# Kernel optimization log

Hardware: AMD Instinct MI355X
Metric: run time of the kernel (lower is better)

Reference implementation:

```python
import jax, jax.numpy as jnp
import numpy as np

N_HEAD = 8
D_K = 64
D_V = 512
TOP_K = 64
NEG = jnp.finfo(jnp.float32).min


def setup_inputs() -> dict:
    key = jax.random.key(0)
    ks = jax.random.split(key, 10)
    B, Lq, Lk, E = 2, 2048, 2048, 512
    q = jax.random.normal(ks[0], (B, Lq, E), dtype=jnp.float32)
    k = jax.random.normal(ks[1], (B, Lk, E), dtype=jnp.float32)
    v = jax.random.normal(ks[2], (B, Lk, D_V), dtype=jnp.float32)
    post_softmax_mask = jax.random.randint(ks[3], (B, 1, Lq, Lk), 0, 2, dtype=jnp.int32)
    query_mask_flat = jax.random.uniform(ks[4], (B, Lq), dtype=jnp.float32)
    # Linear weights stored input-major: y = x @ W
    Wq = jax.random.normal(ks[5], (E, N_HEAD * D_K), dtype=jnp.float32) * (E ** -0.5)
    Wk = jax.random.normal(ks[6], (E, N_HEAD * D_K), dtype=jnp.float32) * (E ** -0.5)
    Wv = jax.random.normal(ks[7], (D_V, N_HEAD * D_V), dtype=jnp.float32) * (D_V ** -0.5)
    Wfc = jax.random.normal(ks[8], (N_HEAD * D_V, D_V), dtype=jnp.float32) * ((N_HEAD * D_V) ** -0.5)
    return {"q": q, "k": k, "v": v, "post_softmax_mask": post_softmax_mask,
            "query_mask_flat": query_mask_flat, "Wq": Wq, "Wk": Wk, "Wv": Wv, "Wfc": Wfc}


def _topk_keep_mask(logits, top_k):
    # Scatter True at the per-row top-k indices (matches torch.topk + scatter_).
    B, H, Lq, Lk = logits.shape
    _, idx = jax.lax.top_k(logits, top_k)              # [B,H,Lq,K]
    rows = B * H * Lq
    keep = jnp.zeros((rows, Lk), dtype=bool)
    keep = keep.at[jnp.arange(rows)[:, None], idx.reshape(rows, top_k)].set(True)
    return keep.reshape(B, H, Lq, Lk)


def reference(q, k, v, post_softmax_mask, query_mask_flat, Wq, Wk, Wv, Wfc):
    B, Lq, _ = q.shape
    Lk = k.shape[1]
    q_proj = (q @ Wq).reshape(B, Lq, N_HEAD, D_K).transpose(0, 2, 1, 3)   # [B,H,Lq,dk]
    k_proj = (k @ Wk).reshape(B, Lk, N_HEAD, D_K).transpose(0, 2, 1, 3)   # [B,H,Lk,dk]
    logits = jnp.einsum('bhqd,bhkd->bhqk', q_proj * (D_K ** -0.5), k_proj).astype(jnp.float32)
    # post-softmax mask (applied pre-softmax via -inf fill, as in source)
    logits = jnp.where(post_softmax_mask == 0, NEG, logits)
    # top-k restriction, skipped for rows where query_mask_flat <= 0.5
    keep = _topk_keep_mask(logits, TOP_K)
    masked_queries = (query_mask_flat > 0.5)[:, None, :, None]            # [B,1,Lq,1]
    keep = jnp.where(masked_queries, keep, True)
    logits = jnp.where(keep, logits, NEG)
    attn_probs = jax.nn.softmax(logits, axis=-1).astype(v.dtype)          # [B,H,Lq,Lk]
    v_proj = (v @ Wv).reshape(B, Lk, N_HEAD, D_V).transpose(0, 2, 1, 3)   # [B,H,Lk,dv]
    mixed = jnp.einsum('bhqk,bhkd->bhqd', attn_probs, v_proj)
    output = mixed.transpose(0, 2, 1, 3).reshape(B, Lq, N_HEAD * D_V) @ Wfc
    return output, attn_probs
```

## Files before the change

### kernel.cpp

```cpp
#include <hip/hip_runtime.h>
#include <stdint.h>

#define NEGF  (-3.402823466e38f)
#define TOPK  64

typedef __attribute__((ext_vector_type(8))) short bfrag8;
typedef __attribute__((ext_vector_type(4))) float f32x4;
typedef __attribute__((ext_vector_type(16))) float f32x16;

static __device__ __forceinline__ unsigned short f2bf(float f) {
  union { float f; unsigned u; } c; c.f = f;
  unsigned u = c.u;
  return (unsigned short)((u + 0x7fffu + ((u >> 16) & 1u)) >> 16);
}
static __device__ __forceinline__ unsigned mono(float x) {
  union { float f; unsigned u; } c; c.f = x;
  return (c.u & 0x80000000u) ? ~c.u : (c.u | 0x80000000u);
}
static __device__ __forceinline__ float invmono(unsigned k) {
  union { unsigned u; float f; } c;
  c.u = (k & 0x80000000u) ? (k ^ 0x80000000u) : ~k;
  return c.f;
}
static __device__ __forceinline__ int waveSum(int v) {
  #pragma unroll
  for (int o = 1; o < 64; o <<= 1) v += __shfl_xor(v, o);
  return v;
}
static __device__ __forceinline__ float waveSumF(float v) {
  #pragma unroll
  for (int o = 1; o < 64; o <<= 1) v += __shfl_xor(v, o);
  return v;
}
static __device__ __forceinline__ unsigned waveMaxU(unsigned v) {
  #pragma unroll
  for (int o = 1; o < 64; o <<= 1) {
    unsigned t = (unsigned)__shfl_xor((int)v, o);
    v = v > t ? v : t;
  }
  return v;
}

template<int OBF>
__global__ __launch_bounds__(256) void transpose_k(const float* __restrict__ in,
                                                   void* __restrict__ out, int R, int C) {
  __shared__ float t[32][33];
  int c0 = blockIdx.x * 32, r0 = blockIdx.y * 32;
  int tx = threadIdx.x & 31, ty = (threadIdx.x >> 5) * 4;
  #pragma unroll
  for (int i = 0; i < 4; i++)
    t[ty + i][tx] = in[(size_t)(r0 + ty + i) * C + c0 + tx];
  __syncthreads();
  #pragma unroll
  for (int i = 0; i < 4; i++) {
    float v = t[tx][ty + i];
    size_t idx = (size_t)(c0 + ty + i) * R + r0 + tx;
    if (OBF) ((unsigned short*)out)[idx] = f2bf(v);
    else     ((float*)out)[idx] = v;
  }
}

__global__ __launch_bounds__(256) void gemm_f32_abt(const float* __restrict__ A,
    const float* __restrict__ Bt, float* __restrict__ C,
    int M, int N, int K, float scale) {
  __shared__ float As[64][65];
  __shared__ float Bs[64][65];
  int tid = threadIdx.x;
  int tx = tid & 15, ty = tid >> 4;
  int m0 = blockIdx.y * 64, n0 = blockIdx.x * 64;
  float acc[4][4] = {};
  for (int k0 = 0; k0 < K; k0 += 64) {
    #pragma unroll
    for (int i = 0; i < 4; i++) {
      int f = tid + (i << 8);
      int row = f >> 4, kc = (f & 15) << 2;
      float4 av = *(const float4*)(A + (size_t)(m0 + row) * K + k0 + kc);
      As[row][kc+0] = av.x; As[row][kc+1] = av.y; As[row][kc+2] = av.z; As[row][kc+3] = av.w;
      float4 bv = *(const float4*)(Bt + (size_t)(n0 + row) * K + k0 + kc);
      Bs[row][kc+0] = bv.x; Bs[row][kc+1] = bv.y; Bs[row][kc+2] = bv.z; Bs[row][kc+3] = bv.w;
    }
    __syncthreads();
    #pragma unroll 4
    for (int d = 0; d < 64; d++) {
      float a[4], b[4];
      #pragma unroll
      for (int i = 0; i < 4; i++) a[i] = As[ty*4 + i][d];
      #pragma unroll
      for (int j = 0; j < 4; j++) b[j] = Bs[tx*4 + j][d];
      #pragma unroll
      for (int i = 0; i < 4; i++)
        #pragma unroll
        for (int j = 0; j < 4; j++)
          acc[i][j] = fmaf(a[i], b[j], acc[i][j]);
    }
    __syncthreads();
  }
  #pragma unroll
  for (int i = 0; i < 4; i++) {
    int m = m0 + ty*4 + i;
    float4 v4;
    v4.x = acc[i][0]*scale; v4.y = acc[i][1]*scale; v4.z = acc[i][2]*scale; v4.w = acc[i][3]*scale;
    int b = m >> 11, l = m & 2047;
    int n = n0 + tx*4;
    int h = n >> 6, dd = n & 63;
    *(float4*)(C + ((((size_t)b*8 + h)*2048 + l)*64 + dd)) = v4;
  }
}

__global__ __launch_bounds__(256) void logits_mask_kernel(
    const float* __restrict__ qp, const float* __restrict__ kp,
    const int* __restrict__ mask, float* __restrict__ out) {
  __shared__ float AsT[64][132];
  __shared__ float BsT[64][132];
  int tid = threadIdx.x;
  int z = blockIdx.z, b = z >> 3;
  int m0 = blockIdx.y * 128, n0 = blockIdx.x * 128;
  const float* Ap = qp + (size_t)z * (2048 * 64);
  const float* Bp = kp + (size_t)z * (2048 * 64);
  {
    int rr = tid >> 2;
    int kq = (tid & 3) << 2;
    #pragma unroll
    for (int pass = 0; pass < 2; pass++) {
      int r = rr + (pass << 6);
      const float* ar = Ap + (size_t)(m0 + r) * 64 + kq;
      const float* br = Bp + (size_t)(n0 + r) * 64 + kq;
      #pragma unroll
      for (int s = 0; s < 4; s++) {
        float4 av = *(const float4*)(ar + (s << 4));
        float4 bv = *(const float4*)(br + (s << 4));
        int k = kq + (s << 4);
        AsT[k+0][r] = av.x; AsT[k+1][r] = av.y; AsT[k+2][r] = av.z; AsT[k+3][r] = av.w;
        BsT[k+0][r] = bv.x; BsT[k+1][r] = bv.y; BsT[k+2][r] = bv.z; BsT[k+3][r] = bv.w;
      }
    }
  }
  __syncthreads();
  int lane = tid & 63, w = tid >> 6;
  int lx = lane & 15, ly = lane >> 4;
  int ra = w * 32 + ly * 4;
  int ca = lx * 4;
  float acc[8][8] = {};
  #pragma unroll 2
  for (int d = 0; d < 64; d++) {
    f32x4 a0 = *(const f32x4*)&AsT[d][ra];
    f32x4 a1 = *(const f32x4*)&AsT[d][ra + 16];
    f32x4 b0 = *(const f32x4*)&BsT[d][ca];
    f32x4 b1 = *(const f32x4*)&BsT[d][ca + 64];
    float a[8] = {a0[0],a0[1],a0[2],a0[3],a1[0],a1[1],a1[2],a1[3]};
    float bb[8] = {b0[0],b0[1],b0[2],b0[3],b1[0],b1[1],b1[2],b1[3]};
    #pragma unroll
    for (int i = 0; i < 8; i++)
      #pragma unroll
      for (int j = 0; j < 8; j++)
        acc[i][j] = fmaf(a[i], bb[j], acc[i][j]);
  }
  size_t outbase = (size_t)z * 2048 * 2048;
  const int* mbase = mask + (size_t)b * 2048 * 2048;
  #pragma unroll
  for (int i = 0; i < 8; i++) {
    int row = m0 + ra + (i & 3) + ((i >> 2) << 4);
    const int* mp = mbase + (size_t)row * 2048 + n0;
    float* op = out + outbase + (size_t)row * 2048 + n0;
    int4 mv0 = *(const int4*)(mp + ca);
    int4 mv1 = *(const int4*)(mp + ca + 64);
    float4 o0, o1;
    o0.x = mv0.x ? acc[i][0] : NEGF;
    o0.y = mv0.y ? acc[i][1] : NEGF;
    o0.z = mv0.z ? acc[i][2] : NEGF;
    o0.w = mv0.w ? acc[i][3] : NEGF;
    o1.x = mv1.x ? acc[i][4] : NEGF;
    o1.y = mv1.y ? acc[i][5] : NEGF;
    o1.z = mv1.z ? acc[i][6] : NEGF;
    o1.w = mv1.w ? acc[i][7] : NEGF;
    *(float4*)(op + ca) = o0;
    *(float4*)(op + ca + 64) = o1;
  }
}

template<typename AT, int MODE>
__global__ __launch_bounds__(256) void gemm_bf16(const AT* __restrict__ A,
    const unsigned short* __restrict__ Bt, void* __restrict__ Cout,
    int M, int N, int K) {
  __shared__ unsigned short As[64][72];
  __shared__ unsigned short Bs[128][72];
  int tid = threadIdx.x;
  int lane = tid & 63, wave = tid >> 6;
  int wr = wave >> 1, wc = wave & 1;
  int m0 = blockIdx.y * 64, n0 = blockIdx.x * 128;
  f32x4 acc[2][4];
  #pragma unroll
  for (int mi = 0; mi < 2; mi++)
    #pragma unroll
    for (int ni = 0; ni < 4; ni++) acc[mi][ni] = (f32x4){0.f, 0.f, 0.f, 0.f};
  int arow = tid >> 2, akc = (tid & 3) << 4;
  int brow = tid >> 1, bkc = (tid & 1) << 5;
  for (int k0 = 0; k0 < K; k0 += 64) {
    {
      const AT* src = A + (size_t)(m0 + arow) * K + k0 + akc;
      if constexpr (sizeof(AT) == 4) {
        const float* s = (const float*)src;
        float4 x0 = *(const float4*)(s + 0);
        float4 x1 = *(const float4*)(s + 4);
        float4 x2 = *(const float4*)(s + 8);
        float4 x3 = *(const float4*)(s + 12);
        union { bfrag8 v; unsigned short u[8]; } p0, p1;
        p0.u[0]=f2bf(x0.x); p0.u[1]=f2bf(x0.y); p0.u[2]=f2bf(x0.z); p0.u[3]=f2bf(x0.w);
        p0.u[4]=f2bf(x1.x); p0.u[5]=f2bf(x1.y); p0.u[6]=f2bf(x1.z); p0.u[7]=f2bf(x1.w);
        p1.u[0]=f2bf(x2.x); p1.u[1]=f2bf(x2.y); p1.u[2]=f2bf(x2.z); p1.u[3]=f2bf(x2.w);
        p1.u[4]=f2bf(x3.x); p1.u[5]=f2bf(x3.y); p1.u[6]=f2bf(x3.z); p1.u[7]=f2bf(x3.w);
        *(bfrag8*)&As[arow][akc + 0] = p0.v;
        *(bfrag8*)&As[arow][akc + 8] = p1.v;
      } else {
        const bfrag8* s = (const bfrag8*)src;
        *(bfrag8*)&As[arow][akc + 0] = s[0];
        *(bfrag8*)&As[arow][akc + 8] = s[1];
      }
    }
    {
      const bfrag8* s = (const bfrag8*)(Bt + (size_t)(n0 + brow) * K + k0 + bkc);
      #pragma unroll
      for (int j = 0; j < 4; j++)
        *(bfrag8*)&Bs[brow][bkc + 8*j] = s[j];
    }
    __syncthreads();
    #pragma unroll
    for (int kh = 0; kh < 2; kh++) {
      int krd = (kh << 5) + ((lane >> 4) << 3);
      bfrag8 af[2], bfr[4];
      #pragma unroll
      for (int mi = 0; mi < 2; mi++)
        af[mi] = *(const bfrag8*)&As[wr*32 + mi*16 + (lane & 15)][krd];
      #pragma unroll
      for (int ni = 0; ni < 4; ni++)
        bfr[ni] = *(const bfrag8*)&Bs[wc*64 + ni*16 + (lane & 15)][krd];
      #pragma unroll
      for (int mi = 0; mi < 2; mi++)
        #pragma unroll
        for (int ni = 0; ni < 4; ni++)
          acc[mi][ni] = __builtin_amdgcn_mfma_f32_16x16x32_bf16(af[mi], bfr[ni], acc[mi][ni], 0, 0, 0);
    }
    __syncthreads();
  }
  #pragma unroll
  for (int mi = 0; mi < 2; mi++) {
    int rb = m0 + wr*32 + mi*16 + ((lane >> 4) << 2);
    #pragma unroll
    for (int ni = 0; ni < 4; ni++) {
      int col = n0 + wc*64 + ni*16 + (lane & 15);
      f32x4 v = acc[mi][ni];
      if (MODE == 0) {
        int b = rb >> 11, l = rb & 2047;
        int h = col >> 9, d = col & 511;
        unsigned short* o = (unsigned short*)Cout + ((((size_t)b*8 + h)*512 + d)*2048 + l);
        ushort4 u;
        u.x = f2bf(v[0]); u.y = f2bf(v[1]); u.z = f2bf(v[2]); u.w = f2bf(v[3]);
        *(ushort4*)o = u;
      } else {
        float* o = (float*)Cout;
        #pragma unroll
        for (int j = 0; j < 4; j++)
          o[(size_t)(rb + j)*512 + col] = v[j];
      }
    }
  }
}

__global__ __launch_bounds__(512) void pv_kernel(const float* __restrict__ probs,
    const unsigned short* __restrict__ vpT, unsigned short* __restrict__ mixed) {
  __shared__ unsigned short As[64][64];
  __shared__ unsigned short Bs[512][64];
  int tid = threadIdx.x;
  int lane = tid & 63, wv = tid >> 6;
  int l31 = lane & 31, lh = lane >> 5;
  int z = blockIdx.z, m0 = blockIdx.y * 64;
  const float* Ap = probs + (size_t)z * 2048 * 2048 + (size_t)m0 * 2048;
  const unsigned short* Bp = vpT + (size_t)z * 512 * 2048;
  f32x16 acc[2][2];
  #pragma unroll
  for (int mf = 0; mf < 2; mf++)
    #pragma unroll
    for (int nf = 0; nf < 2; nf++)
      #pragma unroll
      for (int r = 0; r < 16; r++) acc[mf][nf][r] = 0.f;
  int a_r = tid >> 3, a_c = tid & 7;
  for (int k0 = 0; k0 < 2048; k0 += 64) {
    {
      const float* s = Ap + (size_t)a_r * 2048 + k0 + a_c * 8;
      float4 x0 = *(const float4*)s;
      float4 x1 = *(const float4*)(s + 4);
      union { bfrag8 v; unsigned short u[8]; } p;
      p.u[0]=f2bf(x0.x); p.u[1]=f2bf(x0.y); p.u[2]=f2bf(x0.z); p.u[3]=f2bf(x0.w);
      p.u[4]=f2bf(x1.x); p.u[5]=f2bf(x1.y); p.u[6]=f2bf(x1.z); p.u[7]=f2bf(x1.w);
      *(bfrag8*)&As[a_r][((a_c + a_r) & 7) * 8] = p.v;
    }
    #pragma unroll
    for (int s = 0; s < 8; s++) {
      int n = (tid >> 3) + (s << 6);
      bfrag8 vb = *(const bfrag8*)(Bp + (size_t)n * 2048 + k0 + a_c * 8);
      *(bfrag8*)&Bs[n][((a_c + n) & 7) * 8] = vb;
    }
    __syncthreads();
    #pragma unroll
    for (int ks = 0; ks < 4; ks++) {
      int qd = ks * 2 + lh;
      bfrag8 af[2], bfr[2];
      #pragma unroll
      for (int mf = 0; mf < 2; mf++) {
        int r = mf * 32 + l31;
        af[mf] = *(const bfrag8*)&As[r][((qd + r) & 7) * 8];
      }
      #pragma unroll
      for (int nf = 0; nf < 2; nf++) {
        int n = wv * 64 + nf * 32 + l31;
        bfr[nf] = *(const bfrag8*)&Bs[n][((qd + n) & 7) * 8];
      }
      #pragma unroll
      for (int mf = 0; mf < 2; mf++)
        #pragma unroll
        for (int nf = 0; nf < 2; nf++)
          acc[mf][nf] = __builtin_amdgcn_mfma_f32_32x32x16_bf16(af[mf], bfr[nf], acc[mf][nf], 0, 0, 0);
    }
    __syncthreads();
  }
  int bb = z >> 3, h = z & 7;
  #pragma unroll
  for (int mf = 0; mf < 2; mf++)
    #pragma unroll
    for (int nf = 0; nf < 2; nf++) {
      int n = wv * 64 + nf * 32 + l31;
      #pragma unroll
      for (int r = 0; r < 16; r++) {
        int row = m0 + mf * 32 + (r & 3) + ((r >> 2) << 3) + (lh << 2);
        mixed[((size_t)bb * 2048 + row) * 4096 + h * 512 + n] = f2bf(acc[mf][nf][r]);
      }
    }
}

__global__ __launch_bounds__(256) void topk_softmax_k(float* __restrict__ probs,
    const float* __restrict__ qmaskf) {
  int lane = threadIdx.x & 63;
  int row = blockIdx.x * 4 + (threadIdx.x >> 6);
  int b = row >> 14, q = row & 2047;
  float* rp = probs + (size_t)row * 2048;
  unsigned key[32];
  #pragma unroll
  for (int j = 0; j < 8; j++) {
    int base = (lane << 2) + (j << 8);
    float4 v = *(const float4*)(rp + base);
    key[4*j+0] = mono(v.x);
    key[4*j+1] = mono(v.y);
    key[4*j+2] = mono(v.z);
    key[4*j+3] = mono(v.w);
  }
  unsigned drop = 0;
  bool qm = qmaskf[b * 2048 + q] > 0.5f;
  if (qm) {
    unsigned lo = 0u, hi = 0xFFFFu;
    while (lo < hi) {
      unsigned mid = lo + ((hi - lo + 1u) >> 1);
      unsigned t = mid << 16;
      int c = 0;
      #pragma unroll
      for (int e = 0; e < 32; e++) c += (key[e] >= t) ? 1 : 0;
      c = waveSum(c);
      if (c >= TOPK) lo = mid; else hi = mid - 1u;
    }
    unsigned P = lo;
    unsigned hiMax = (P << 16) | 0xFFFFu;
    int cgt_hi = 0;
    #pragma unroll
    for (int e = 0; e < 32; e++) cgt_hi += (key[e] > hiMax) ? 1 : 0;
    cgt_hi = waveSum(cgt_hi);
    int remaining = TOPK - cgt_hi;
    unsigned cur = 0xFFFFFFFFu;
    unsigned K64 = P << 16;
    for (;;) {
      unsigned mx = 0;
      #pragma unroll
      for (int e = 0; e < 32; e++) {
        unsigned kk = key[e];
        if ((kk >> 16) == P && kk < cur) mx = mx > kk ? mx : kk;
      }
      mx = waveMaxU(mx);
      int ce = 0;
      #pragma unroll
      for (int e = 0; e < 32; e++) ce += (key[e] == mx) ? 1 : 0;
      ce = waveSum(ce);
      if (remaining <= ce) { K64 = mx; break; }
      remaining -= ce;
      cur = mx;
    }
    int cgt = 0, ceq = 0;
    #pragma unroll
    for (int e = 0; e < 32; e++) { cgt += (key[e] > K64) ? 1 : 0; ceq += (key[e] == K64) ? 1 : 0; }
    cgt = waveSum(cgt);
    int ceqT = waveSum(ceq);
    int r = TOPK - cgt;
    #pragma unroll
    for (int e = 0; e < 32; e++) if (key[e] < K64) drop |= (1u << e);
    if (ceqT > r) {
      int taken = 0;
      for (int j = 0; j < 8; j++) {
        int cl = 0, eqm = 0;
        #pragma unroll
        for (int t = 0; t < 4; t++)
          if (key[4*j+t] == K64) { eqm |= (1 << t); cl++; }
        int incl = cl;
        for (int o = 1; o < 64; o <<= 1) {
          int tt = __shfl_up(incl, o);
          if (lane >= o) incl += tt;
        }
        int pref = incl - cl;
        int tot = __shfl(incl, 63);
        int rk = taken + pref;
        #pragma unroll
        for (int t = 0; t < 4; t++) {
          if ((eqm >> t) & 1) {
            if (rk >= r) drop |= (1u << (4*j+t));
            rk++;
          }
        }
        taken += tot;
      }
    }
  }
  unsigned kmax = 0;
  #pragma unroll
  for (int e = 0; e < 32; e++)
    if (!((drop >> e) & 1u)) kmax = kmax > key[e] ? kmax : key[e];
  kmax = waveMaxU(kmax);
  float mx = invmono(kmax);
  float ex[32]; float s = 0.f;
  #pragma unroll
  for (int e = 0; e < 32; e++) {
    float t = ((drop >> e) & 1u) ? 0.f : __expf(invmono(key[e]) - mx);
    ex[e] = t; s += t;
  }
  s = waveSumF(s);
  float inv = 1.0f / s;
  #pragma unroll
  for (int j = 0; j < 8; j++) {
    int base = (lane << 2) + (j << 8);
    float4 o;
    o.x = ex[4*j+0]*inv; o.y = ex[4*j+1]*inv; o.z = ex[4*j+2]*inv; o.w = ex[4*j+3]*inv;
    *(float4*)(rp + base) = o;
  }
}

extern "C" void kernel_launch(void* const* d_in, const int* in_sizes, int n_in,
                              void* d_out, int out_size, void* d_ws, size_t ws_size,
                              hipStream_t stream) {
  (void)in_sizes; (void)n_in; (void)out_size; (void)ws_size;
  const float* q     = (const float*)d_in[0];
  const float* k     = (const float*)d_in[1];
  const float* v     = (const float*)d_in[2];
  const int*   mask  = (const int*)d_in[3];
  const float* qmask = (const float*)d_in[4];
  const float* Wq    = (const float*)d_in[5];
  const float* Wk    = (const float*)d_in[6];
  const float* Wv    = (const float*)d_in[7];
  const float* Wfc   = (const float*)d_in[8];

  float* out   = (float*)d_out;
  float* probs = out + 2097152;

  char* ws = (char*)d_ws;
  float*          qp    = (float*)(ws + 0);
  float*          kp    = (float*)(ws + 8388608);
  unsigned short* vpT   = (unsigned short*)(ws + 16777216);
  unsigned short* mixed = (unsigned short*)(ws + 50331648);
  float*          WqT   = (float*)(ws + 83886080);
  float*          WkT   = (float*)(ws + 84934656);
  unsigned short* WvT   = (unsigned short*)(ws + 85983232);
  unsigned short* WfcT  = (unsigned short*)(ws + 90177536);

  transpose_k<0><<<dim3(16, 16),  256, 0, stream>>>(Wq,  WqT,  512, 512);
  transpose_k<0><<<dim3(16, 16),  256, 0, stream>>>(Wk,  WkT,  512, 512);
  transpose_k<1><<<dim3(128, 16), 256, 0, stream>>>(Wv,  WvT,  512, 4096);
  transpose_k<1><<<dim3(16, 128), 256, 0, stream>>>(Wfc, WfcT, 4096, 512);

  gemm_f32_abt<<<dim3(8, 64), 256, 0, stream>>>(q, WqT, qp, 4096, 512, 512, 0.125f);
  gemm_f32_abt<<<dim3(8, 64), 256, 0, stream>>>(k, WkT, kp, 4096, 512, 512, 1.0f);

  gemm_bf16<float, 0><<<dim3(32, 64), 256, 0, stream>>>(v, WvT, vpT, 4096, 4096, 512);

  logits_mask_kernel<<<dim3(16, 16, 16), 256, 0, stream>>>(qp, kp, mask, probs);

  topk_softmax_k<<<dim3(8192), 256, 0, stream>>>(probs, qmask);

  pv_kernel<<<dim3(1, 32, 16), 512, 0, stream>>>(probs, vpT, mixed);

  gemm_bf16<unsigned short, 2><<<dim3(4, 64), 256, 0, stream>>>(mixed, WfcT, out, 4096, 512, 4096);
}
```

Measured before the change: 588.7 us.

## Merge Q/K projections into one larger-tile kernel and rewrite V projection with 32x32 MFMA

Replaces the two separate fp32 Q and K projection launches with a single kernel that handles both via blockIdx.z. It uses 128x128 tiles with an 8x8 per-thread register block and transposed shared-memory staging. The V projection gets its own kernel that computes the transposed output directly with 32x32x16 bf16 MFMA, 128x128 tiles and XOR-style swizzled shared memory. The aim is more arithmetic per load and fewer launches, but the V output stores are scalar and strided, which may cost bandwidth.

```diff
diff --git a/kernel.cpp b/kernel.cpp
--- a/kernel.cpp
+++ b/kernel.cpp
@@ -60,50 +60,67 @@
   }
 }
 
-__global__ __launch_bounds__(256) void gemm_f32_abt(const float* __restrict__ A,
-    const float* __restrict__ Bt, float* __restrict__ C,
-    int M, int N, int K, float scale) {
-  __shared__ float As[64][65];
-  __shared__ float Bs[64][65];
+__global__ __launch_bounds__(256) void proj_f32_kernel(
+    const float* __restrict__ q, const float* __restrict__ k,
+    const float* __restrict__ WqT, const float* __restrict__ WkT,
+    float* __restrict__ qp, float* __restrict__ kp) {
+  __shared__ float AsT[64][132];
+  __shared__ float BsT[64][132];
   int tid = threadIdx.x;
-  int tx = tid & 15, ty = tid >> 4;
-  int m0 = blockIdx.y * 64, n0 = blockIdx.x * 64;
-  float acc[4][4] = {};
-  for (int k0 = 0; k0 < K; k0 += 64) {
-    #pragma unroll
-    for (int i = 0; i < 4; i++) {
-      int f = tid + (i << 8);
-      int row = f >> 4, kc = (f & 15) << 2;
-      float4 av = *(const float4*)(A + (size_t)(m0 + row) * K + k0 + kc);
-      As[row][kc+0] = av.x; As[row][kc+1] = av.y; As[row][kc+2] = av.z; As[row][kc+3] = av.w;
-      float4 bv = *(const float4*)(Bt + (size_t)(n0 + row) * K + k0 + kc);
-      Bs[row][kc+0] = bv.x; Bs[row][kc+1] = bv.y; Bs[row][kc+2] = bv.z; Bs[row][kc+3] = bv.w;
-    }
-    __syncthreads();
-    #pragma unroll 4
+  int z = blockIdx.z;
+  const float* A  = z ? k : q;
+  const float* Bt = z ? WkT : WqT;
+  float* out      = z ? kp : qp;
+  float scale     = z ? 1.0f : 0.125f;
+  int m0 = blockIdx.y * 128, n0 = blockIdx.x * 128;
+  int lane = tid & 63, w = tid >> 6;
+  int lx = lane & 15, ly = lane >> 4;
+  int ra = w * 32 + ly * 4;
+  int ca = lx * 4;
+  int rr = tid >> 1;
+  int kq0 = (tid & 1) << 5;
+  float acc[8][8] = {};
+  for (int k0 = 0; k0 < 512; k0 += 64) {
+    const float* ar = A  + (size_t)(m0 + rr) * 512 + k0 + kq0;
+    const float* br = Bt + (size_t)(n0 + rr) * 512 + k0 + kq0;
+    #pragma unroll
+    for (int s = 0; s < 8; s++) {
+      float4 av = *(const float4*)(ar + (s << 2));
+      float4 bv = *(const float4*)(br + (s << 2));
+      int kk = kq0 + (s << 2);
+      AsT[kk+0][rr] = av.x; AsT[kk+1][rr] = av.y; AsT[kk+2][rr] = av.z; AsT[kk+3][rr] = av.w;
+      BsT[kk+0][rr] = bv.x; BsT[kk+1][rr] = bv.y; BsT[kk+2][rr] = bv.z; BsT[kk+3][rr] = bv.w;
+    }
+    __syncthreads();
+    #pragma unroll 2
     for (int d = 0; d < 64; d++) {
-      float a[4], b[4];
-      #pragma unroll
-      for (int i = 0; i < 4; i++) a[i] = As[ty*4 + i][d];
-      #pragma unroll
-      for (int j = 0; j < 4; j++) b[j] = Bs[tx*4 + j][d];
-      #pragma unroll
-      for (int i = 0; i < 4; i++)
+      f32x4 a0 = *(const f32x4*)&AsT[d][ra];
+      f32x4 a1 = *(const f32x4*)&AsT[d][ra + 16];
+      f32x4 b0 = *(const f32x4*)&BsT[d][ca];
+      f32x4 b1 = *(const f32x4*)&BsT[d][ca + 64];
+      float a[8] = {a0[0],a0[1],a0[2],a0[3],a1[0],a1[1],a1[2],a1[3]};
+      float bb[8] = {b0[0],b0[1],b0[2],b0[3],b1[0],b1[1],b1[2],b1[3]};
+      #pragma unroll
+      for (int i = 0; i < 8; i++)
         #pragma unroll
-        for (int j = 0; j < 4; j++)
-          acc[i][j] = fmaf(a[i], b[j], acc[i][j]);
-    }
-    __syncthreads();
-  }
-  #pragma unroll
-  for (int i = 0; i < 4; i++) {
-    int m = m0 + ty*4 + i;
-    float4 v4;
-    v4.x = acc[i][0]*scale; v4.y = acc[i][1]*scale; v4.z = acc[i][2]*scale; v4.w = acc[i][3]*scale;
+        for (int j = 0; j < 8; j++)
+          acc[i][j] = fmaf(a[i], bb[j], acc[i][j]);
+    }
+    __syncthreads();
+  }
+  #pragma unroll
+  for (int i = 0; i < 8; i++) {
+    int m = m0 + ra + (i & 3) + ((i >> 2) << 4);
     int b = m >> 11, l = m & 2047;
-    int n = n0 + tx*4;
-    int h = n >> 6, dd = n & 63;
-    *(float4*)(C + ((((size_t)b*8 + h)*2048 + l)*64 + dd)) = v4;
+    #pragma unroll
+    for (int half = 0; half < 2; half++) {
+      int n = n0 + ca + half * 64;
+      int h = n >> 6, dd = n & 63;
+      float4 v4;
+      v4.x = acc[i][half*4+0]*scale; v4.y = acc[i][half*4+1]*scale;
+      v4.z = acc[i][half*4+2]*scale; v4.w = acc[i][half*4+3]*scale;
+      *(float4*)(out + ((((size_t)b*8 + h)*2048 + l)*64 + dd)) = v4;
+    }
   }
 }
 
@@ -178,9 +195,87 @@
   }
 }
 
-template<typename AT, int MODE>
-__global__ __launch_bounds__(256) void gemm_bf16(const AT* __restrict__ A,
-    const unsigned short* __restrict__ Bt, void* __restrict__ Cout,
+__global__ __launch_bounds__(256) void vproj_kernel(const float* __restrict__ v,
+    const unsigned short* __restrict__ WvT, unsigned short* __restrict__ vpT) {
+  __shared__ unsigned short As[128][64];
+  __shared__ unsigned short Bs[128][64];
+  int tid = threadIdx.x;
+  int lane = tid & 63, wv = tid >> 6;
+  int l31 = lane & 31, lh = lane >> 5;
+  int wr = wv >> 1, wc = wv & 1;
+  int z = blockIdx.z, b = z >> 3, h = z & 7;
+  int m0 = blockIdx.y * 128, n0 = blockIdx.x * 128;
+  const unsigned short* Ap = WvT + (size_t)(h * 512 + m0) * 512;
+  const float* Bp = v + ((size_t)b * 2048 + n0) * 512;
+  f32x16 acc[2][2];
+  #pragma unroll
+  for (int mf = 0; mf < 2; mf++)
+    #pragma unroll
+    for (int nf = 0; nf < 2; nf++)
+      #pragma unroll
+      for (int r = 0; r < 16; r++) acc[mf][nf][r] = 0.f;
+  int srow = tid >> 1;
+  int skc = (tid & 1) << 5;
+  for (int k0 = 0; k0 < 512; k0 += 64) {
+    {
+      const bfrag8* s = (const bfrag8*)(Ap + (size_t)srow * 512 + k0 + skc);
+      #pragma unroll
+      for (int j = 0; j < 4; j++) {
+        int c = (skc >> 3) + j;
+        *(bfrag8*)&As[srow][((c + srow) & 7) * 8] = s[j];
+      }
+    }
+    {
+      const float* s = Bp + (size_t)srow * 512 + k0 + skc;
+      #pragma unroll
+      for (int j = 0; j < 4; j++) {
+        float4 x0 = *(const float4*)(s + 8*j);
+        float4 x1 = *(const float4*)(s + 8*j + 4);
+        union { bfrag8 v; unsigned short u[8]; } p;
+        p.u[0]=f2bf(x0.x); p.u[1]=f2bf(x0.y); p.u[2]=f2bf(x0.z); p.u[3]=f2bf(x0.w);
+        p.u[4]=f2bf(x1.x); p.u[5]=f2bf(x1.y); p.u[6]=f2bf(x1.z); p.u[7]=f2bf(x1.w);
+        int c = (skc >> 3) + j;
+        *(bfrag8*)&Bs[srow][((c + srow) & 7) * 8] = p.v;
+      }
+    }
+    __syncthreads();
+    #pragma unroll
+    for (int ks = 0; ks < 4; ks++) {
+      int qd = ks * 2 + lh;
+      bfrag8 af[2], bfr[2];
+      #pragma unroll
+      for (int mf = 0; mf < 2; mf++) {
+        int r = wr * 64 + mf * 32 + l31;
+        af[mf] = *(const bfrag8*)&As[r][((qd + r) & 7) * 8];
+      }
+      #pragma unroll
+      for (int nf = 0; nf < 2; nf++) {
+        int n = wc * 64 + nf * 32 + l31;
+        bfr[nf] = *(const bfrag8*)&Bs[n][((qd + n) & 7) * 8];
+      }
+      #pragma unroll
+      for (int mf = 0; mf < 2; mf++)
+        #pragma unroll
+        for (int nf = 0; nf < 2; nf++)
+          acc[mf][nf] = __builtin_amdgcn_mfma_f32_32x32x16_bf16(af[mf], bfr[nf], acc[mf][nf], 0, 0, 0);
+    }
+    __syncthreads();
+  }
+  #pragma unroll
+  for (int mf = 0; mf < 2; mf++)
+    #pragma unroll
+    for (int nf = 0; nf < 2; nf++) {
+      int l = n0 + wc * 64 + nf * 32 + l31;
+      #pragma unroll
+      for (int r = 0; r < 16; r++) {
+        int d = m0 + wr * 64 + mf * 32 + (r & 3) + ((r >> 2) << 3) + (lh << 2);
+        vpT[((size_t)z * 512 + d) * 2048 + l] = f2bf(acc[mf][nf][r]);
+      }
+    }
+}
+
+__global__ __launch_bounds__(256) void gemm_bf16_fc(const unsigned short* __restrict__ A,
+    const unsigned short* __restrict__ Bt, float* __restrict__ Cout,
     int M, int N, int K) {
   __shared__ unsigned short As[64][72];
   __shared__ unsigned short Bs[128][72];
@@ -197,25 +292,9 @@
   int brow = tid >> 1, bkc = (tid & 1) << 5;
   for (int k0 = 0; k0 < K; k0 += 64) {
     {
-      const AT* src = A + (size_t)(m0 + arow) * K + k0 + akc;
-      if constexpr (sizeof(AT) == 4) {
-        const float* s = (const float*)src;
-        float4 x0 = *(const float4*)(s + 0);
-        float4 x1 = *(const float4*)(s + 4);
-        float4 x2 = *(const float4*)(s + 8);
-        float4 x3 = *(const float4*)(s + 12);
-        union { bfrag8 v; unsigned short u[8]; } p0, p1;
-        p0.u[0]=f2bf(x0.x); p0.u[1]=f2bf(x0.y); p0.u[2]=f2bf(x0.z); p0.u[3]=f2bf(x0.w);
-        p0.u[4]=f2bf(x1.x); p0.u[5]=f2bf(x1.y); p0.u[6]=f2bf(x1.z); p0.u[7]=f2bf(x1.w);
-        p1.u[0]=f2bf(x2.x); p1.u[1]=f2bf(x2.y); p1.u[2]=f2bf(x2.z); p1.u[3]=f2bf(x2.w);
-        p1.u[4]=f2bf(x3.x); p1.u[5]=f2bf(x3.y); p1.u[6]=f2bf(x3.z); p1.u[7]=f2bf(x3.w);
-        *(bfrag8*)&As[arow][akc + 0] = p0.v;
-        *(bfrag8*)&As[arow][akc + 8] = p1.v;
-      } else {
-        const bfrag8* s = (const bfrag8*)src;
-        *(bfrag8*)&As[arow][akc + 0] = s[0];
-        *(bfrag8*)&As[arow][akc + 8] = s[1];
-      }
+      const bfrag8* s = (const bfrag8*)(A + (size_t)(m0 + arow) * K + k0 + akc);
+      *(bfrag8*)&As[arow][akc + 0] = s[0];
+      *(bfrag8*)&As[arow][akc + 8] = s[1];
     }
     {
       const bfrag8* s = (const bfrag8*)(Bt + (size_t)(n0 + brow) * K + k0 + bkc);
@@ -249,19 +328,9 @@
     for (int ni = 0; ni < 4; ni++) {
       int col = n0 + wc*64 + ni*16 + (lane & 15);
       f32x4 v = acc[mi][ni];
-      if (MODE == 0) {
-        int b = rb >> 11, l = rb & 2047;
-        int h = col >> 9, d = col & 511;
-        unsigned short* o = (unsigned short*)Cout + ((((size_t)b*8 + h)*512 + d)*2048 + l);
-        ushort4 u;
-        u.x = f2bf(v[0]); u.y = f2bf(v[1]); u.z = f2bf(v[2]); u.w = f2bf(v[3]);
-        *(ushort4*)o = u;
-      } else {
-        float* o = (float*)Cout;
-        #pragma unroll
-        for (int j = 0; j < 4; j++)
-          o[(size_t)(rb + j)*512 + col] = v[j];
-      }
+      #pragma unroll
+      for (int j = 0; j < 4; j++)
+        Cout[(size_t)(rb + j)*512 + col] = v[j];
     }
   }
 }
@@ -480,10 +549,9 @@
   transpose_k<1><<<dim3(128, 16), 256, 0, stream>>>(Wv,  WvT,  512, 4096);
   transpose_k<1><<<dim3(16, 128), 256, 0, stream>>>(Wfc, WfcT, 4096, 512);
 
-  gemm_f32_abt<<<dim3(8, 64), 256, 0, stream>>>(q, WqT, qp, 4096, 512, 512, 0.125f);
-  gemm_f32_abt<<<dim3(8, 64), 256, 0, stream>>>(k, WkT, kp, 4096, 512, 512, 1.0f);
-
-  gemm_bf16<float, 0><<<dim3(32, 64), 256, 0, stream>>>(v, WvT, vpT, 4096, 4096, 512);
+  proj_f32_kernel<<<dim3(4, 32, 2), 256, 0, stream>>>(q, k, WqT, WkT, qp, kp);
+
+  vproj_kernel<<<dim3(16, 4, 16), 256, 0, stream>>>(v, WvT, vpT);
 
   logits_mask_kernel<<<dim3(16, 16, 16), 256, 0, stream>>>(qp, kp, mask, probs);
 
@@ -491,5 +559,5 @@
 
   pv_kernel<<<dim3(1, 32, 16), 512, 0, stream>>>(probs, vpT, mixed);
 
-  gemm_bf16<unsigned short, 2><<<dim3(4, 64), 256, 0, stream>>>(mixed, WfcT, out, 4096, 512, 4096);
-}
+  gemm_bf16_fc<<<dim3(4, 64), 256, 0, stream>>>(mixed, WfcT, out, 4096, 512, 4096);
+}
```

After: 581.0 us. About the same (-1.3%).
